# Kernel optimization log

Hardware: AMD Instinct MI355X
Metric: run time of the kernel (lower is better)

## Reference

```python
import jax, jax.numpy as jnp
import numpy as np

N_NODES = 50000
N_EDGES = 800000
NODE_F = 5
EDGE_F = 4
HID = 128


def _glorot(key, shape):
    fan_in, fan_out = shape[0], shape[1]
    lim = float(np.sqrt(6.0 / (fan_in + fan_out)))
    return jax.random.uniform(key, shape, jnp.float32, -lim, lim)


def setup_inputs() -> dict:
    key = jax.random.key(0)
    ks = jax.random.split(key, 12)
    x = jax.random.normal(ks[0], (N_NODES, NODE_F), jnp.float32)
    edge_attr = jax.random.normal(ks[1], (N_EDGES, EDGE_F), jnp.float32)
    edge_index = jax.random.randint(ks[2], (2, N_EDGES), 0, N_NODES, jnp.int64)
    return {
        "x": x,
        "edge_attr": edge_attr,
        "W1": _glorot(ks[3], (NODE_F, HID)),
        "b1": jnp.zeros((HID,), jnp.float32),
        "W2": _glorot(ks[4], (HID, HID)),
        "b2": jnp.zeros((HID,), jnp.float32),
        "Wm1": _glorot(ks[5], (2 * HID + EDGE_F, HID)),
        "bm1": jnp.zeros((HID,), jnp.float32),
        "Wm2": _glorot(ks[6], (HID, 1)),
        "bm2": jnp.zeros((1,), jnp.float32),
        "edge_index": edge_index,
    }


def _gcn_conv(x, W, b, row, col, norm, n_nodes):
    # GCNConv: out = D^{-1/2} (A + I) D^{-1/2} X W + b
    xw = x @ W                                   # [N, H]
    msg = norm[:, None] * xw[row]                # [E+N, H] gather + scale
    agg = jax.ops.segment_sum(msg, col, num_segments=n_nodes)
    return agg + b


def reference(x, edge_attr, W1, b1, W2, b2, Wm1, bm1, Wm2, bm2, edge_index):
    n = x.shape[0]
    src, dst = edge_index[0], edge_index[1]
    # add self-loops (PyG GCNConv default)
    loop = jnp.arange(n, dtype=edge_index.dtype)
    row = jnp.concatenate([src, loop])
    col = jnp.concatenate([dst, loop])
    # symmetric normalization, in-degree w/ self-loops
    deg = jax.ops.segment_sum(jnp.ones_like(col, dtype=x.dtype), col, num_segments=n)
    dis = jnp.where(deg > 0, jax.lax.rsqrt(deg), 0.0)
    norm = dis[row] * dis[col]

    h = jax.nn.relu(_gcn_conv(x, W1, b1, row, col, norm, n))
    h = _gcn_conv(h, W2, b2, row, col, norm, n)

    # gather-concat edge MLP
    edge_emb = jnp.concatenate([h[src], h[dst], edge_attr], axis=1)  # [E, 2H+F]
    out = jax.nn.relu(edge_emb @ Wm1 + bm1) @ Wm2 + bm2              # [E, 1]
    return jax.nn.sigmoid(out[:, 0])
```

## Files before the change

kernel.cpp:

```cpp
#include <hip/hip_runtime.h>
#include <math.h>

#define HID 128
typedef unsigned int uint;
typedef __attribute__((ext_vector_type(8))) __bf16 bf16x8;
typedef __attribute__((ext_vector_type(4))) float f32x4;
typedef __attribute__((ext_vector_type(2))) float f32x2;


__device__ __forceinline__ uint pack_bf2(float x, float y) {
    union { float f; uint u; } a, b;
    a.f = x; b.f = y;
    uint lo = (a.u + 0x7fffu + ((a.u >> 16) & 1u)) >> 16;
    uint hi = (b.u + 0x7fffu + ((b.u >> 16) & 1u)) & 0xffff0000u;
    return lo | hi;
}

__device__ __forceinline__ unsigned short bf16r(float x) {
    union { float f; uint u; } a; a.f = x;
    return (unsigned short)((a.u + 0x7fffu + ((a.u >> 16) & 1u)) >> 16);
}

__device__ __forceinline__ f32x2 bf2f(uint v) {
    union { uint u[2]; f32x2 f; } r;
    r.u[0] = v << 16;
    r.u[1] = v & 0xffff0000u;
    return r.f;
}

__device__ __forceinline__ f32x2 mk2(float s) { f32x2 r; r.x = s; r.y = s; return r; }
__device__ __forceinline__ f32x2 max2z(f32x2 a) {
    f32x2 r; r.x = fmaxf(a.x, 0.f); r.y = fmaxf(a.y, 0.f); return r;
}

template<int CTRL>
__device__ __forceinline__ float dpp_add(float x) {
    union { float f; int i; } u, r;
    u.f = x;
    r.i = __builtin_amdgcn_update_dpp(0, u.i, CTRL, 0xf, 0xf, true);
    return x + r.f;
}


__global__ void prep_kernel(const float* __restrict__ W2, const float* __restrict__ Wm1,
                            const float* __restrict__ b2, const float* __restrict__ bm1,
                            uint* __restrict__ fWc, float* __restrict__ brow) {
    int t0 = blockIdx.x * blockDim.x + threadIdx.x;
    if (t0 < 65536) {
        int ks = t0 & 3;
        int i = t0 >> 2;
        int p = i & 3, lane = (i >> 2) & 63, kk = (i >> 8) & 3, ct = i >> 10;
        int k = kk * 32 + (lane >> 4) * 8 + p * 2;
        int n2 = ct * 16 + (lane & 15);
        const float* wmc = (n2 < 128) ? (Wm1 + n2) : (Wm1 + 128 * HID + (n2 - 128));
        const float* w2r0 = W2 + (size_t)k * HID + ks * 32;
        const float* w2r1 = w2r0 + HID;
        const float* wm = wmc + (size_t)(ks * 32) * HID;
        float d0 = 0.f, d1 = 0.f;
        #pragma unroll 8
        for (int j = 0; j < 32; ++j) {
            float w = wm[(size_t)j * HID];
            d0 += w2r0[j] * w;
            d1 += w2r1[j] * w;
        }
        d0 = dpp_add<0xB1>(d0); d0 = dpp_add<0x4E>(d0);
        d1 = dpp_add<0xB1>(d1); d1 = dpp_add<0x4E>(d1);
        if (ks == 0) fWc[i] = pack_bf2(d0, d1);
    } else if (t0 < 65536 + 1024) {
        int r = t0 - 65536;
        int ks = r & 3;
        int i = r >> 2;
        const float* wmc = (i < 128) ? (Wm1 + i) : (Wm1 + 128 * HID + (i - 128));
        float d = 0.f;
        for (int j = ks * 32; j < ks * 32 + 32; ++j) d += b2[j] * wmc[(size_t)j * HID];
        d = dpp_add<0xB1>(d); d = dpp_add<0x4E>(d);
        if (ks == 0) brow[i] = d + ((i < 128) ? bm1[i] : 0.f);
    }
}

__global__ void hist_rank(const int* __restrict__ dst, int* __restrict__ cnt,
                          int* __restrict__ rank, int E) {
    int e = blockIdx.x * blockDim.x + threadIdx.x;
    if (e < E) rank[e] = atomicAdd(&cnt[dst[e]], 1);
}

__global__ void scan1(const int* __restrict__ cnt, int* __restrict__ excl,
                      int* __restrict__ bsum, int N) {
    __shared__ int sh[256];
    int tid = threadIdx.x;
    int gid = blockIdx.x * 256 + tid;
    int v = (gid < N) ? cnt[gid] : 0;
    sh[tid] = v;
    __syncthreads();
    for (int o = 1; o < 256; o <<= 1) {
        int t = (tid >= o) ? sh[tid - o] : 0;
        __syncthreads();
        sh[tid] += t;
        __syncthreads();
    }
    if (gid < N) excl[gid] = sh[tid] - v;
    if (tid == 255) bsum[blockIdx.x] = sh[255];
}

__global__ void scan3x(const int* __restrict__ cnt, int* __restrict__ rowptr,
                       const int* __restrict__ bsum,
                       float* __restrict__ dis, const float* __restrict__ x,
                       uint4* __restrict__ xps, int N, int E, int NB) {
    __shared__ int sh[256];
    __shared__ int ex[256];
    int tid = threadIdx.x;
    int v = (tid < NB) ? bsum[tid] : 0;
    sh[tid] = v;
    __syncthreads();
    for (int o = 1; o < 256; o <<= 1) {
        int t = (tid >= o) ? sh[tid - o] : 0;
        __syncthreads();
        sh[tid] += t;
        __syncthreads();
    }
    ex[tid] = sh[tid] - v;
    __syncthreads();
    int gid = blockIdx.x * 256 + tid;
    if (gid < N) {
        rowptr[gid] = rowptr[gid] + ex[blockIdx.x];
        float dn = rsqrtf((float)cnt[gid] + 1.0f);
        dis[gid] = dn;
        const float* xr = x + (size_t)gid * 5;
        uint4 pk;
        pk.x = pack_bf2(dn * xr[0], dn * xr[1]);
        pk.y = pack_bf2(dn * xr[2], dn * xr[3]);
        pk.z = pack_bf2(dn * xr[4], 0.f);
        pk.w = 0u;
        xps[gid] = pk;
    }
    if (gid == N) rowptr[N] = E;
}

__global__ void scatter2(const int* __restrict__ src, const int* __restrict__ dst,
                         const int* __restrict__ rowptr, const int* __restrict__ rank,
                         uint2* __restrict__ csr2, int E) {
    int e = blockIdx.x * blockDim.x + threadIdx.x;
    if (e < E) {
        int d = dst[e];
        int pos = rowptr[d] + rank[e];
        csr2[pos] = make_uint2((uint)src[e] | ((uint)d << 16), (uint)e);
    }
}

__launch_bounds__(256)
__global__ void layer1_kernel(const uint4* __restrict__ xps, const uint2* __restrict__ csr2,
                              const int* __restrict__ rowptr, const float* __restrict__ dis,
                              const float* __restrict__ W1, const float* __restrict__ b1,
                              uint* __restrict__ hs1, int N) {
    __shared__ float sW[5 * HID];
    __shared__ float sb[HID];
    int tid = threadIdx.x;
    for (int i = tid; i < 5 * HID; i += 256) sW[i] = W1[i];
    for (int i = tid; i < HID; i += 256) sb[i] = b1[i];
    __syncthreads();

    int sub = tid & 3;
    int n = blockIdx.x * 64 + (tid >> 2);
    if (n >= N) return;
    int beg = rowptr[n], end = rowptr[n + 1];
    float a0 = 0.f, a1 = 0.f, a2 = 0.f, a3 = 0.f, a4 = 0.f;
    for (int i = beg + sub; i < end; i += 4) {
        uint s = csr2[i].x & 0xffffu;
        uint4 v = xps[s];
        f32x2 v01 = bf2f(v.x), v23 = bf2f(v.y), v4 = bf2f(v.z);
        a0 += v01.x; a1 += v01.y; a2 += v23.x; a3 += v23.y; a4 += v4.x;
    }
    a0 = dpp_add<0xB1>(a0); a0 = dpp_add<0x4E>(a0);
    a1 = dpp_add<0xB1>(a1); a1 = dpp_add<0x4E>(a1);
    a2 = dpp_add<0xB1>(a2); a2 = dpp_add<0x4E>(a2);
    a3 = dpp_add<0xB1>(a3); a3 = dpp_add<0x4E>(a3);
    a4 = dpp_add<0xB1>(a4); a4 = dpp_add<0x4E>(a4);
    {
        uint4 v = xps[n];
        f32x2 v01 = bf2f(v.x), v23 = bf2f(v.y), v4 = bf2f(v.z);
        a0 += v01.x; a1 += v01.y; a2 += v23.x; a3 += v23.y; a4 += v4.x;
    }
    float dn = dis[n];
    a0 *= dn; a1 *= dn; a2 *= dn; a3 *= dn; a4 *= dn;

    uint* op = hs1 + (size_t)n * 64;
    #pragma unroll
    for (int p = 0; p < 16; ++p) {
        int q = p * 4 + sub;
        int j = q * 2;
        float t0 = sb[j]     + a0 * sW[j]     + a1 * sW[HID + j]     + a2 * sW[2*HID + j]
                             + a3 * sW[3*HID + j] + a4 * sW[4*HID + j];
        float t1 = sb[j + 1] + a0 * sW[j + 1] + a1 * sW[HID + j + 1] + a2 * sW[2*HID + j + 1]
                             + a3 * sW[3*HID + j + 1] + a4 * sW[4*HID + j + 1];
        op[q] = pack_bf2(fmaxf(t0, 0.f) * dn, fmaxf(t1, 0.f) * dn);
    }
}

__launch_bounds__(256)
__global__ void agg_gemm(const uint4* __restrict__ hs1, const uint2* __restrict__ csr2,
                         const int* __restrict__ rowptr, const float* __restrict__ dis,
                         const uint4* __restrict__ Bf, const float* __restrict__ brow,
                         unsigned short* __restrict__ out, int N) {
    __shared__ uint gt[16][64];
    int wave = threadIdx.x >> 6, lane = threadIdx.x & 63;
    int gl = lane & 15, grp = lane >> 4;
    int nb = blockIdx.x * 16;
    int r0 = nb + wave * 4;

    int rp[5];
    #pragma unroll
    for (int j = 0; j < 5; ++j) {
        int idx = r0 + j;
        rp[j] = rowptr[(idx <= N) ? idx : N];
    }

    for (int q = 0; q < 4; ++q) {
        int r = wave * 4 + q;
        int n = nb + r;
        if (n < N) {
            int beg = rp[q], end = rp[q + 1];
            f32x2 acc[4];
            #pragma unroll
            for (int p = 0; p < 4; ++p) acc[p] = mk2(0.f);
            for (int base = beg + grp; base < end; base += 16) {
                int i1 = base + 4, i2 = base + 8, i3 = base + 12;
                uint s0 = csr2[base].x & 0xffffu;
                uint s1 = csr2[(i1 < end) ? i1 : beg].x & 0xffffu;
                uint s2 = csr2[(i2 < end) ? i2 : beg].x & 0xffffu;
                uint s3 = csr2[(i3 < end) ? i3 : beg].x & 0xffffu;
                uint4 v0 = hs1[(s0 << 4) + (uint)gl];
                uint4 v1 = hs1[(s1 << 4) + (uint)gl];
                uint4 v2 = hs1[(s2 << 4) + (uint)gl];
                uint4 v3 = hs1[(s3 << 4) + (uint)gl];
                f32x2 w1 = mk2((i1 < end) ? 1.f : 0.f);
                f32x2 w2 = mk2((i2 < end) ? 1.f : 0.f);
                f32x2 w3 = mk2((i3 < end) ? 1.f : 0.f);
                acc[0] += bf2f(v0.x);  acc[1] += bf2f(v0.y);
                acc[2] += bf2f(v0.z);  acc[3] += bf2f(v0.w);
                acc[0] += bf2f(v1.x) * w1;  acc[1] += bf2f(v1.y) * w1;
                acc[2] += bf2f(v1.z) * w1;  acc[3] += bf2f(v1.w) * w1;
                acc[0] += bf2f(v2.x) * w2;  acc[1] += bf2f(v2.y) * w2;
                acc[2] += bf2f(v2.z) * w2;  acc[3] += bf2f(v2.w) * w2;
                acc[0] += bf2f(v3.x) * w3;  acc[1] += bf2f(v3.y) * w3;
                acc[2] += bf2f(v3.z) * w3;  acc[3] += bf2f(v3.w) * w3;
            }
            #pragma unroll
            for (int p = 0; p < 4; ++p) {
                f32x2 t;
                t.x = __shfl_xor(acc[p].x, 16, 64); t.y = __shfl_xor(acc[p].y, 16, 64);
                acc[p] += t;
                t.x = __shfl_xor(acc[p].x, 32, 64); t.y = __shfl_xor(acc[p].y, 32, 64);
                acc[p] += t;
            }
            if (grp == 0) {
                uint4 sv = hs1[((uint)n << 4) + (uint)gl];
                f32x2 dn = mk2(dis[n]);
                f32x2 o0 = (acc[0] + bf2f(sv.x)) * dn;
                f32x2 o1 = (acc[1] + bf2f(sv.y)) * dn;
                f32x2 o2 = (acc[2] + bf2f(sv.z)) * dn;
                f32x2 o3 = (acc[3] + bf2f(sv.w)) * dn;
                gt[r][gl * 4]     = pack_bf2(o0.x, o0.y);
                gt[r][gl * 4 + 1] = pack_bf2(o1.x, o1.y);
                gt[r][gl * 4 + 2] = pack_bf2(o2.x, o2.y);
                gt[r][gl * 4 + 3] = pack_bf2(o3.x, o3.y);
            }
        } else if (grp == 0) {
            gt[r][gl * 4] = 0; gt[r][gl * 4 + 1] = 0;
            gt[r][gl * 4 + 2] = 0; gt[r][gl * 4 + 3] = 0;
        }
    }
    __syncthreads();

    int quad = lane >> 4;
    bf16x8 afr[4];
    #pragma unroll
    for (int kk = 0; kk < 4; ++kk)
        afr[kk] = *(const bf16x8*)&gt[gl][kk * 16 + quad * 4];

    for (int cc = 0; cc < 4; ++cc) {
        int c = wave * 4 + cc;
        f32x4 acc = {0.f, 0.f, 0.f, 0.f};
        #pragma unroll
        for (int kk = 0; kk < 4; ++kk) {
            bf16x8 bfr = *(const bf16x8*)&Bf[(size_t)(c * 4 + kk) * 64 + lane];
            acc = __builtin_amdgcn_mfma_f32_16x16x32_bf16(afr[kk], bfr, acc, 0, 0, 0);
        }
        float bv = brow[c * 16 + gl];
        #pragma unroll
        for (int reg = 0; reg < 4; ++reg) {
            int row = nb + quad * 4 + reg;
            if (row < N)
                out[(size_t)row * 256 + c * 16 + gl] = bf16r(acc[reg] + bv);
        }
    }
}

__launch_bounds__(256)
__global__ void edge_mlp_kernel(const uint4* __restrict__ HsHd, const float4* __restrict__ ea,
                                const uint2* __restrict__ csr2,
                                const float* __restrict__ Wb, const float* __restrict__ Wm2,
                                const float* __restrict__ bm2,
                                float* __restrict__ out, int E) {
    int lane = threadIdx.x & 63;
    int gl = lane & 15, grp = lane >> 4;

    f32x2 wb[4][4], w2[4];
    #pragma unroll
    for (int k = 0; k < 4; ++k) {
        const f32x2* wp = (const f32x2*)(Wb + k * HID + gl * 8);
        #pragma unroll
        for (int p = 0; p < 4; ++p) wb[k][p] = wp[p];
    }
    {
        const f32x2* wp = (const f32x2*)(Wm2 + gl * 8);
        #pragma unroll
        for (int p = 0; p < 4; ++p) w2[p] = wp[p];
    }
    float b2v = bm2[0];

    int gwave = (blockIdx.x * blockDim.x + threadIdx.x) >> 6;
    int nw = (gridDim.x * blockDim.x) >> 6;
    int stride = nw * 16;
    int base = gwave * 16;
    if (base >= E) return;

    uint2 ce[4];
    #pragma unroll
    for (int t = 0; t < 4; ++t) {
        int i = base + grp * 4 + t;
        ce[t] = csr2[(i < E) ? i : 0];
    }

    while (base < E) {
        int nbase = base + stride;

        uint4 hv[4], dv[4];
        float4 eav[4];
        uint eid[4];
        #pragma unroll
        for (int t = 0; t < 4; ++t) {
            uint cx = ce[t].x;
            eid[t] = ce[t].y;
            hv[t] = HsHd[((cx & 0xffffu) << 5) + (uint)gl];
            dv[t] = HsHd[((cx >> 16) << 5) + 16u + (uint)gl];
            eav[t] = ea[eid[t]];
        }

        if (nbase < E) {
            #pragma unroll
            for (int t = 0; t < 4; ++t) {
                int i = nbase + grp * 4 + t;
                ce[t] = csr2[(i < E) ? i : 0];
            }
        }

        float pr[4];
        #pragma unroll
        for (int t = 0; t < 4; ++t) {
            uint hu[4] = {hv[t].x, hv[t].y, hv[t].z, hv[t].w};
            uint du[4] = {dv[t].x, dv[t].y, dv[t].z, dv[t].w};
            f32x2 e0 = mk2(eav[t].x), e1 = mk2(eav[t].y);
            f32x2 e2 = mk2(eav[t].z), e3 = mk2(eav[t].w);
            f32x2 p2 = mk2(0.f);
            #pragma unroll
            for (int p = 0; p < 4; ++p) {
                f32x2 tt = bf2f(hu[p]) + bf2f(du[p]);
                tt += e0 * wb[0][p];
                tt += e1 * wb[1][p];
                tt += e2 * wb[2][p];
                tt += e3 * wb[3][p];
                tt = max2z(tt);
                p2 += tt * w2[p];
            }
            pr[t] = p2.x + p2.y;
        }
        #pragma unroll
        for (int t = 0; t < 4; ++t) {
            float s = pr[t];
            s = dpp_add<0xB1>(s);
            s = dpp_add<0x4E>(s);
            s = dpp_add<0x124>(s);
            s = dpp_add<0x128>(s);
            pr[t] = s;
        }
        if (gl == 0) {
            #pragma unroll
            for (int t = 0; t < 4; ++t) {
                int i = base + grp * 4 + t;
                if (i < E)
                    out[eid[t]] = 1.f / (1.f + exp2f(-1.44269504f * (pr[t] + b2v)));
            }
        }
        base = nbase;
    }
}


extern "C" void kernel_launch(void* const* d_in, const int* in_sizes, int n_in,
                              void* d_out, int out_size, void* d_ws, size_t ws_size,
                              hipStream_t stream) {
    const float* x    = (const float*)d_in[0];
    const float* ea   = (const float*)d_in[1];
    const float* W1   = (const float*)d_in[2];
    const float* b1   = (const float*)d_in[3];
    const float* W2   = (const float*)d_in[4];
    const float* b2   = (const float*)d_in[5];
    const float* Wm1  = (const float*)d_in[6];
    const float* bm1  = (const float*)d_in[7];
    const float* Wm2  = (const float*)d_in[8];
    const float* bm2  = (const float*)d_in[9];
    const int*   ei   = (const int*)d_in[10];

    const int N = in_sizes[0] / 5;
    const int E = in_sizes[1] / 4;
    const int* src = ei;
    const int* dst = ei + E;
    float* out = (float*)d_out;

    char* ws = (char*)d_ws;
    size_t off = 0;
    auto alloc = [&](size_t bytes) -> void* {
        void* p = ws + off;
        off = (off + bytes + 255) & ~(size_t)255;
        return p;
    };
    int*    cnt    = (int*)alloc((size_t)N * 4);
    int*    rowptr = (int*)alloc((size_t)(N + 1) * 4);
    int*    bsum   = (int*)alloc(256 * 4);
    float*  dis    = (float*)alloc((size_t)N * 4);
    int*    rank   = (int*)alloc((size_t)(E + 8) * 4);
    uint2*  csr2   = (uint2*)alloc((size_t)(E + 8) * 8);
    uint4*  xps    = (uint4*)alloc((size_t)N * 16);
    uint*   hs1    = (uint*)alloc((size_t)N * 64 * 4);
    uint*   HsHd   = (uint*)alloc((size_t)N * 128 * 4);
    uint*   fWc    = (uint*)alloc(16384 * 4);
    float*  brow   = (float*)alloc(256 * 4);
    (void)ws_size; (void)n_in; (void)out_size;

    const int NB = (N + 255) / 256;
    const int EB = (E + 255) / 256;

    hipMemsetAsync(cnt, 0, (size_t)N * 4, stream);
    prep_kernel<<<260, 256, 0, stream>>>(W2, Wm1, b2, bm1, fWc, brow);
    hist_rank<<<EB, 256, 0, stream>>>(dst, cnt, rank, E);
    scan1<<<NB, 256, 0, stream>>>(cnt, rowptr, bsum, N);
    scan3x<<<NB, 256, 0, stream>>>(cnt, rowptr, bsum, dis, x, xps, N, E, NB);
    scatter2<<<EB, 256, 0, stream>>>(src, dst, rowptr, rank, csr2, E);

    layer1_kernel<<<(N + 63) / 64, 256, 0, stream>>>(xps, csr2, rowptr, dis, W1, b1, hs1, N);

    agg_gemm<<<(N + 15) / 16, 256, 0, stream>>>((const uint4*)hs1, csr2, rowptr, dis,
                                                (const uint4*)fWc, brow,
                                                (unsigned short*)HsHd, N);

    edge_mlp_kernel<<<2048, 256, 0, stream>>>((const uint4*)HsHd, (const float4*)ea, csr2,
                                              Wm1 + 256 * HID, Wm2, bm2, out, E);
}
```

Before: 252.5 us.

## Permute edge attributes into CSR order and restructure neighbor aggregation per row

The scatter kernel now also writes edge attributes in CSR order, so the edge MLP reads them sequentially instead of gathering by edge id, when workspace allows. The agg_gemm gather is reorganised so each 16-lane group owns one node row, prefetching CSR entries, and padded lanes read a zeroed dummy row N instead of using masked weights. This removes cross-group shuffle reductions and the serial per-row loop, at the cost of an extra E*16-byte write and possible load imbalance across rows of differing degree.

```diff
diff --git a/kernel.cpp b/kernel.cpp
--- a/kernel.cpp
+++ b/kernel.cpp
@@ -3,6 +3,7 @@
 
 #define HID 128
 typedef unsigned int uint;
+typedef unsigned short u16;
 typedef __attribute__((ext_vector_type(8))) __bf16 bf16x8;
 typedef __attribute__((ext_vector_type(4))) float f32x4;
 typedef __attribute__((ext_vector_type(2))) float f32x2;
@@ -138,12 +139,15 @@
 
 __global__ void scatter2(const int* __restrict__ src, const int* __restrict__ dst,
                          const int* __restrict__ rowptr, const int* __restrict__ rank,
-                         uint2* __restrict__ csr2, int E) {
+                         const float4* __restrict__ ea,
+                         uint2* __restrict__ csr2, float4* __restrict__ ear,
+                         int use_ear, int E) {
     int e = blockIdx.x * blockDim.x + threadIdx.x;
     if (e < E) {
         int d = dst[e];
         int pos = rowptr[d] + rank[e];
         csr2[pos] = make_uint2((uint)src[e] | ((uint)d << 16), (uint)e);
+        if (use_ear) ear[pos] = ea[e];
     }
 }
 
@@ -157,6 +161,10 @@
     int tid = threadIdx.x;
     for (int i = tid; i < 5 * HID; i += 256) sW[i] = W1[i];
     for (int i = tid; i < HID; i += 256) sb[i] = b1[i];
+    if (blockIdx.x == 0 && tid < 16) {
+        uint4 z; z.x = 0u; z.y = 0u; z.z = 0u; z.w = 0u;
+        ((uint4*)hs1)[(size_t)N * 16 + tid] = z;
+    }
     __syncthreads();
 
     int sub = tid & 3;
@@ -202,73 +210,58 @@
                          const uint4* __restrict__ Bf, const float* __restrict__ brow,
                          unsigned short* __restrict__ out, int N) {
     __shared__ uint gt[16][64];
-    int wave = threadIdx.x >> 6, lane = threadIdx.x & 63;
+    int tid = threadIdx.x;
+    int wave = tid >> 6, lane = tid & 63;
     int gl = lane & 15, grp = lane >> 4;
     int nb = blockIdx.x * 16;
-    int r0 = nb + wave * 4;
-
-    int rp[5];
-    #pragma unroll
-    for (int j = 0; j < 5; ++j) {
-        int idx = r0 + j;
-        rp[j] = rowptr[(idx <= N) ? idx : N];
-    }
-
-    for (int q = 0; q < 4; ++q) {
-        int r = wave * 4 + q;
-        int n = nb + r;
-        if (n < N) {
-            int beg = rp[q], end = rp[q + 1];
-            f32x2 acc[4];
+    int r = wave * 4 + grp;
+    int n = nb + r;
+    const uint* cxp = (const uint*)csr2;
+
+    f32x2 acc0 = mk2(0.f), acc1 = mk2(0.f), acc2 = mk2(0.f), acc3 = mk2(0.f);
+    float dn = 0.f;
+    if (n < N) {
+        dn = dis[n];
+        int beg = rowptr[n], end = rowptr[n + 1];
+        int i = beg;
+        if (i < end) {
+            int lst = end - 1;
+            uint cb[4];
             #pragma unroll
-            for (int p = 0; p < 4; ++p) acc[p] = mk2(0.f);
-            for (int base = beg + grp; base < end; base += 16) {
-                int i1 = base + 4, i2 = base + 8, i3 = base + 12;
-                uint s0 = csr2[base].x & 0xffffu;
-                uint s1 = csr2[(i1 < end) ? i1 : beg].x & 0xffffu;
-                uint s2 = csr2[(i2 < end) ? i2 : beg].x & 0xffffu;
-                uint s3 = csr2[(i3 < end) ? i3 : beg].x & 0xffffu;
-                uint4 v0 = hs1[(s0 << 4) + (uint)gl];
-                uint4 v1 = hs1[(s1 << 4) + (uint)gl];
-                uint4 v2 = hs1[(s2 << 4) + (uint)gl];
-                uint4 v3 = hs1[(s3 << 4) + (uint)gl];
-                f32x2 w1 = mk2((i1 < end) ? 1.f : 0.f);
-                f32x2 w2 = mk2((i2 < end) ? 1.f : 0.f);
-                f32x2 w3 = mk2((i3 < end) ? 1.f : 0.f);
-                acc[0] += bf2f(v0.x);  acc[1] += bf2f(v0.y);
-                acc[2] += bf2f(v0.z);  acc[3] += bf2f(v0.w);
-                acc[0] += bf2f(v1.x) * w1;  acc[1] += bf2f(v1.y) * w1;
-                acc[2] += bf2f(v1.z) * w1;  acc[3] += bf2f(v1.w) * w1;
-                acc[0] += bf2f(v2.x) * w2;  acc[1] += bf2f(v2.y) * w2;
-                acc[2] += bf2f(v2.z) * w2;  acc[3] += bf2f(v2.w) * w2;
-                acc[0] += bf2f(v3.x) * w3;  acc[1] += bf2f(v3.y) * w3;
-                acc[2] += bf2f(v3.z) * w3;  acc[3] += bf2f(v3.w) * w3;
+            for (int t = 0; t < 4; ++t) {
+                int a = i + t; a = (a > lst) ? lst : a;
+                cb[t] = cxp[(size_t)a * 2];
             }
-            #pragma unroll
-            for (int p = 0; p < 4; ++p) {
-                f32x2 t;
-                t.x = __shfl_xor(acc[p].x, 16, 64); t.y = __shfl_xor(acc[p].y, 16, 64);
-                acc[p] += t;
-                t.x = __shfl_xor(acc[p].x, 32, 64); t.y = __shfl_xor(acc[p].y, 32, 64);
-                acc[p] += t;
+            while (i < end) {
+                uint s0 = (i     < end) ? (cb[0] & 0xffffu) : (uint)N;
+                uint s1 = (i + 1 < end) ? (cb[1] & 0xffffu) : (uint)N;
+                uint s2 = (i + 2 < end) ? (cb[2] & 0xffffu) : (uint)N;
+                uint s3 = (i + 3 < end) ? (cb[3] & 0xffffu) : (uint)N;
+                #pragma unroll
+                for (int t = 0; t < 4; ++t) {
+                    int a = i + 4 + t; a = (a > lst) ? lst : a;
+                    cb[t] = cxp[(size_t)a * 2];
+                }
+                uint4 v0 = hs1[(size_t)s0 * 16 + gl];
+                uint4 v1 = hs1[(size_t)s1 * 16 + gl];
+                uint4 v2 = hs1[(size_t)s2 * 16 + gl];
+                uint4 v3 = hs1[(size_t)s3 * 16 + gl];
+                acc0 += bf2f(v0.x); acc1 += bf2f(v0.y); acc2 += bf2f(v0.z); acc3 += bf2f(v0.w);
+                acc0 += bf2f(v1.x); acc1 += bf2f(v1.y); acc2 += bf2f(v1.z); acc3 += bf2f(v1.w);
+                acc0 += bf2f(v2.x); acc1 += bf2f(v2.y); acc2 += bf2f(v2.z); acc3 += bf2f(v2.w);
+                acc0 += bf2f(v3.x); acc1 += bf2f(v3.y); acc2 += bf2f(v3.z); acc3 += bf2f(v3.w);
+                i += 4;
             }
-            if (grp == 0) {
-                uint4 sv = hs1[((uint)n << 4) + (uint)gl];
-                f32x2 dn = mk2(dis[n]);
-                f32x2 o0 = (acc[0] + bf2f(sv.x)) * dn;
-                f32x2 o1 = (acc[1] + bf2f(sv.y)) * dn;
-                f32x2 o2 = (acc[2] + bf2f(sv.z)) * dn;
-                f32x2 o3 = (acc[3] + bf2f(sv.w)) * dn;
-                gt[r][gl * 4]     = pack_bf2(o0.x, o0.y);
-                gt[r][gl * 4 + 1] = pack_bf2(o1.x, o1.y);
-                gt[r][gl * 4 + 2] = pack_bf2(o2.x, o2.y);
-                gt[r][gl * 4 + 3] = pack_bf2(o3.x, o3.y);
-            }
-        } else if (grp == 0) {
-            gt[r][gl * 4] = 0; gt[r][gl * 4 + 1] = 0;
-            gt[r][gl * 4 + 2] = 0; gt[r][gl * 4 + 3] = 0;
-        }
-    }
+        }
+        {
+            uint4 sv = hs1[(size_t)n * 16 + gl];
+            acc0 += bf2f(sv.x); acc1 += bf2f(sv.y); acc2 += bf2f(sv.z); acc3 += bf2f(sv.w);
+        }
+    }
+    gt[r][gl * 4 + 0] = pack_bf2(acc0.x * dn, acc0.y * dn);
+    gt[r][gl * 4 + 1] = pack_bf2(acc1.x * dn, acc1.y * dn);
+    gt[r][gl * 4 + 2] = pack_bf2(acc2.x * dn, acc2.y * dn);
+    gt[r][gl * 4 + 3] = pack_bf2(acc3.x * dn, acc3.y * dn);
     __syncthreads();
 
     int quad = lane >> 4;
@@ -296,7 +289,9 @@
 }
 
 __launch_bounds__(256)
-__global__ void edge_mlp_kernel(const uint4* __restrict__ HsHd, const float4* __restrict__ ea,
+__global__ void edge_mlp_kernel(const uint4* __restrict__ HsHd,
+                                const float4* __restrict__ ea,
+                                const float4* __restrict__ ear, int use_ear,
                                 const uint2* __restrict__ csr2,
                                 const float* __restrict__ Wb, const float* __restrict__ Wm2,
                                 const float* __restrict__ bm2,
@@ -341,9 +336,11 @@
         for (int t = 0; t < 4; ++t) {
             uint cx = ce[t].x;
             eid[t] = ce[t].y;
+            int i = base + grp * 4 + t;
+            int j = (i < E) ? i : 0;
             hv[t] = HsHd[((cx & 0xffffu) << 5) + (uint)gl];
             dv[t] = HsHd[((cx >> 16) << 5) + 16u + (uint)gl];
-            eav[t] = ea[eid[t]];
+            eav[t] = use_ear ? ear[j] : ea[eid[t]];
         }
 
         if (nbase < E) {
@@ -431,11 +428,13 @@
     int*    rank   = (int*)alloc((size_t)(E + 8) * 4);
     uint2*  csr2   = (uint2*)alloc((size_t)(E + 8) * 8);
     uint4*  xps    = (uint4*)alloc((size_t)N * 16);
-    uint*   hs1    = (uint*)alloc((size_t)N * 64 * 4);
+    uint*   hs1    = (uint*)alloc((size_t)(N + 1) * 64 * 4);
     uint*   HsHd   = (uint*)alloc((size_t)N * 128 * 4);
     uint*   fWc    = (uint*)alloc(16384 * 4);
     float*  brow   = (float*)alloc(256 * 4);
-    (void)ws_size; (void)n_in; (void)out_size;
+    float4* ear    = (float4*)alloc((size_t)(E + 8) * 16);
+    int use_ear = (off <= ws_size) ? 1 : 0;
+    (void)n_in; (void)out_size;
 
     const int NB = (N + 255) / 256;
     const int EB = (E + 255) / 256;
@@ -445,7 +444,8 @@
     hist_rank<<<EB, 256, 0, stream>>>(dst, cnt, rank, E);
     scan1<<<NB, 256, 0, stream>>>(cnt, rowptr, bsum, N);
     scan3x<<<NB, 256, 0, stream>>>(cnt, rowptr, bsum, dis, x, xps, N, E, NB);
-    scatter2<<<EB, 256, 0, stream>>>(src, dst, rowptr, rank, csr2, E);
+    scatter2<<<EB, 256, 0, stream>>>(src, dst, rowptr, rank, (const float4*)ea,
+                                     csr2, ear, use_ear, E);
 
     layer1_kernel<<<(N + 63) / 64, 256, 0, stream>>>(xps, csr2, rowptr, dis, W1, b1, hs1, N);
 
@@ -453,6 +453,8 @@
                                                 (const uint4*)fWc, brow,
                                                 (unsigned short*)HsHd, N);
 
-    edge_mlp_kernel<<<2048, 256, 0, stream>>>((const uint4*)HsHd, (const float4*)ea, csr2,
+    edge_mlp_kernel<<<2048, 256, 0, stream>>>((const uint4*)HsHd,
+                                              (const float4*)ea, (const float4*)ear,
+                                              use_ear, csr2,
                                               Wm1 + 256 * HID, Wm2, bm2, out, E);
 }
```

Result: no change. 249.5 us (-1.2%).
